# Kernel tuning notes

Measured on AMD Instinct MI355X. Metric: run time of the kernel, lower is better.

## Reference

```python
import jax, jax.numpy as jnp
import numpy as np

S, N, D, F = 32, 128, 256, 516
TRI = (N - 1) * N // 2  # fact(n-1) = n(n-1)/2 lower-triangular edge slots


def _mlp_readout(y, W0, b0, W1, b1, W2, b2):
    # standard MLPReadout with L=2 halving layers + final linear
    y = jax.nn.relu(y @ W0.T + b0)
    y = jax.nn.relu(y @ W1.T + b1)
    return y @ W2.T + b2


def _gru(xs, h0, Wih, Whh, bih, bhh):
    # xs: (S, T, Din); torch.nn.GRUCell math, scanned over time
    def step(h, x_t):
        gi = x_t @ Wih.T + bih
        gh = h @ Whh.T + bhh
        i_r, i_z, i_n = jnp.split(gi, 3, axis=-1)
        h_r, h_z, h_n = jnp.split(gh, 3, axis=-1)
        r = jax.nn.sigmoid(i_r + h_r)
        z = jax.nn.sigmoid(i_z + h_z)
        n = jnp.tanh(i_n + r * h_n)
        h_new = (1.0 - z) * n + z * h
        return h_new, h_new
    _, out = jax.lax.scan(step, h0, jnp.swapaxes(xs, 0, 1))
    return jnp.swapaxes(out, 0, 1)  # (S, T, D)


def setup_inputs() -> dict:
    key = jax.random.key(0)
    ks = jax.random.split(key, 16)
    def nrm(k, shape, s=0.05):
        return (jax.random.normal(k, shape) * s).astype(jnp.float32)
    return {
        'x': jax.random.uniform(ks[0], (S, N, F), dtype=jnp.float32),
        'con': jax.random.uniform(ks[1], (S, TRI, 2), dtype=jnp.float32),
        'z_ph': jax.random.uniform(ks[2], (D,), minval=-1.0, maxval=1.0, dtype=jnp.float32),
        'init_ph': jax.random.uniform(ks[3], (D,), minval=-1.0, maxval=1.0, dtype=jnp.float32),
        'cc_W0': nrm(ks[4], (D, 2 * D)), 'cc_b0': jnp.zeros((D,), jnp.float32),
        'cc_W1': nrm(ks[5], (D // 2, D)), 'cc_b1': jnp.zeros((D // 2,), jnp.float32),
        'cc_W2': nrm(ks[6], (D, D // 2)), 'cc_b2': jnp.zeros((D,), jnp.float32),
        'er_W0': nrm(ks[7], (D, 2 * D)), 'er_b0': jnp.zeros((D,), jnp.float32),
        'er_W1': nrm(ks[8], (D // 2, D)), 'er_b1': jnp.zeros((D // 2,), jnp.float32),
        'er_W2': nrm(ks[9], (2, D // 2)), 'er_b2': jnp.zeros((2,), jnp.float32),
        'rr_W': nrm(ks[10], (D, F)), 'rr_b': jnp.zeros((D,), jnp.float32),
        'dec_Wih': nrm(ks[11], (3 * D, D)), 'dec_Whh': nrm(ks[12], (3 * D, D)),
        'dec_bih': jnp.zeros((3 * D,), jnp.float32), 'dec_bhh': jnp.zeros((3 * D,), jnp.float32),
        'upd_Wih': nrm(ks[13], (3 * D, D)), 'upd_Whh': nrm(ks[14], (3 * D, D)),
        'upd_bih': jnp.zeros((3 * D,), jnp.float32), 'upd_bhh': jnp.zeros((3 * D,), jnp.float32),
    }


def reference(x, con, z_ph, init_ph, cc_W0, cc_b0, cc_W1, cc_b1, cc_W2, cc_b2,
              er_W0, er_b0, er_W1, er_b1, er_W2, er_b2, rr_W, rr_b,
              dec_Wih, dec_Whh, dec_bih, dec_bhh, upd_Wih, upd_Whh, upd_bih, upd_bhh):
    Sb = x.shape[0]
    Nm1 = x.shape[1] - 1
    # initial content = compact_content([z ; init]) (same for every sample)
    c0 = _mlp_readout(jnp.concatenate([z_ph, init_ph])[None, :],
                      cc_W0, cc_b0, cc_W1, cc_b1, cc_W2, cc_b2)
    c0 = jnp.broadcast_to(c0, (Sb, D))
    # update-model input stream depends only on data x[:, 1:] -> precompute
    rnninp = jax.nn.relu(jnp.einsum('snf,df->snd', x[:, 1:], rr_W) + rr_b)  # (S, N-1, D)
    h0 = jnp.zeros((Sb, D), x.dtype)
    u_out = _gru(rnninp, h0, upd_Wih, upd_Whh, upd_bih, upd_bhh)            # (S, N-1, D)
    # decoder consumes content0 then the first N-2 update outputs
    content_seq = jnp.concatenate([c0[:, None], u_out[:, :-1]], axis=1)     # (S, N-1, D)
    mem = _gru(content_seq, h0, dec_Wih, dec_Whh, dec_bih, dec_bhh)         # (S, N-1, D)
    # step i emits edges (j, i) for j <= i; flatten lower triangle (static indices)
    i_idx = np.repeat(np.arange(Nm1), np.arange(1, Nm1 + 1))
    j_idx = np.concatenate([np.arange(i + 1) for i in range(Nm1)])
    edge_rep = jnp.concatenate([mem[:, j_idx], mem[:, i_idx]], axis=-1)     # (S, TRI, 2D)
    logits = _mlp_readout(edge_rep, er_W0, er_b0, er_W1, er_b1, er_W2, er_b2)
    p = jax.nn.softmax(logits, axis=-1)                                     # (S, TRI, 2)
    # F.binary_cross_entropy with torch's log clamp at -100
    bce = -(con * jnp.clip(jnp.log(p), -100.0, None)
            + (1.0 - con) * jnp.clip(jnp.log1p(-p), -100.0, None))
    return jnp.sum(bce, axis=1)  # (S, 2) negative log-likelihood per class slot
```

## Files before the change

### kernel.cpp

```cpp
#include <hip/hip_runtime.h>
#include <cstddef>

#define S_ 32
#define NM1 127
#define D_ 256
#define F_ 516
#define TRI_ 8128
#define G_ 768
#define M_ (S_ * NM1)

typedef __bf16 v8bf __attribute__((ext_vector_type(8)));
typedef float v4f __attribute__((ext_vector_type(4)));

__device__ __forceinline__ unsigned short f2bf(float f) {
    unsigned int u = __float_as_uint(f);
    unsigned int r = (u + 0x7FFFu + ((u >> 16) & 1u)) >> 16;
    return (unsigned short)r;
}

__device__ __forceinline__ void store4bf(unsigned short* p, float4 v) {
    ushort4 q;
    q.x = f2bf(v.x); q.y = f2bf(v.y); q.z = f2bf(v.z); q.w = f2bf(v.w);
    *(ushort4*)p = q;
}

__device__ __forceinline__ v8bf u4_to_v8bf(uint4 u) {
    union { uint4 u; v8bf v; } x; x.u = u; return x.v;
}

__device__ __forceinline__ float sigmoidf_(float x) { return 1.f / (1.f + __expf(-x)); }

__device__ __forceinline__ float fast_tanh(float x) {
    float ax = fabsf(x);
    float e = __expf(2.f * ax);
    float t = 1.f - 2.f / (e + 1.f);
    return copysignf(t, x);
}

__global__ __launch_bounds__(1024) void c0_kernel(
    const float* __restrict__ z_ph, const float* __restrict__ init_ph,
    const float* __restrict__ W0, const float* __restrict__ b0,
    const float* __restrict__ W1, const float* __restrict__ b1,
    const float* __restrict__ W2, const float* __restrict__ b2,
    float* __restrict__ c0_out, float* __restrict__ out_zero)
{
    __shared__ float v[512];
    __shared__ float h0[256];
    __shared__ float h1[128];
    __shared__ float red[4][256];
    __shared__ float red1[8][128];
    const int t = threadIdx.x;
    if (t < 512) v[t] = (t < 256) ? z_ph[t] : init_ph[t - 256];
    if (t < 64) out_zero[t] = 0.f;
    __syncthreads();
    {
        int row = t & 255, part = t >> 8;
        const float* w = W0 + (size_t)row * 512 + part * 128;
        const float* vv = v + part * 128;
        float a = 0.f;
        for (int k = 0; k < 128; ++k) a += w[k] * vv[k];
        red[part][row] = a;
    }
    __syncthreads();
    if (t < 256) {
        float a = b0[t] + red[0][t] + red[1][t] + red[2][t] + red[3][t];
        h0[t] = fmaxf(a, 0.f);
    }
    __syncthreads();
    {
        int row = t & 127, part = t >> 7;
        const float* w = W1 + (size_t)row * 256 + part * 32;
        const float* vv = h0 + part * 32;
        float a = 0.f;
        for (int k = 0; k < 32; ++k) a += w[k] * vv[k];
        red1[part][row] = a;
    }
    __syncthreads();
    if (t < 128) {
        float a = b1[t];
        for (int p = 0; p < 8; ++p) a += red1[p][t];
        h1[t] = fmaxf(a, 0.f);
    }
    __syncthreads();
    {
        int row = t & 255, part = t >> 8;
        const float* w = W2 + (size_t)row * 128 + part * 32;
        const float* vv = h1 + part * 32;
        float a = 0.f;
        for (int k = 0; k < 32; ++k) a += w[k] * vv[k];
        red[part][row] = a;
    }
    __syncthreads();
    if (t < 256) c0_out[t] = b2[t] + red[0][t] + red[1][t] + red[2][t] + red[3][t];
}

__device__ __forceinline__ void do_packfrag(const float* __restrict__ W,
                                            uint4* __restrict__ wbuf, int idx)
{
    if (idx >= 48 * 8 * 64) return;
    int ct = idx >> 9;
    int rem = idx & 511;
    int kk = rem >> 6;
    int lane = rem & 63;
    int lr = lane & 15, quad = lane >> 4;
    const float* src = W + (size_t)(ct * 16 + lr) * 256 + kk * 32 + quad * 8;
    unsigned int wd[4];
#pragma unroll
    for (int i = 0; i < 4; ++i)
        wd[i] = (unsigned int)f2bf(src[2 * i]) | ((unsigned int)f2bf(src[2 * i + 1]) << 16);
    uint4 v; v.x = wd[0]; v.y = wd[1]; v.z = wd[2]; v.w = wd[3];
    wbuf[idx] = v;
}

__device__ __forceinline__ void do_cvt(const float* __restrict__ src,
                                       unsigned short* __restrict__ dst,
                                       int idx, int N, int K, int lds_, int off, int ldd)
{
    if (idx >= N * ldd) return;
    int n = idx / ldd, k = idx - n * ldd;
    float v = (k < K) ? src[(size_t)n * lds_ + off + k] : 0.f;
    dst[idx] = f2bf(v);
}

#define PREP_BLOCKS 2888

__global__ __launch_bounds__(256) void prep_all(
    const float* __restrict__ upd_Whh, uint4* __restrict__ wfU,
    const float* __restrict__ dec_Whh, uint4* __restrict__ wfD,
    const float* __restrict__ rr_W, unsigned short* __restrict__ rwbf,
    const float* __restrict__ upd_Wih, unsigned short* __restrict__ uwbf,
    const float* __restrict__ dec_Wih, unsigned short* __restrict__ dwbf,
    const float* __restrict__ er_W0, unsigned short* __restrict__ w0bf,
    const float* __restrict__ er_W1, unsigned short* __restrict__ w1bf)
{
    int bid = blockIdx.x;
    const int tid = threadIdx.x;
    if (bid < 96) { do_packfrag(upd_Whh, wfU, bid * 256 + tid); return; }
    bid -= 96;
    if (bid < 96) { do_packfrag(dec_Whh, wfD, bid * 256 + tid); return; }
    bid -= 96;
    if (bid < 520) { do_cvt(rr_W, rwbf, bid * 256 + tid, 256, 516, 516, 0, 520); return; }
    bid -= 520;
    if (bid < 768) { do_cvt(upd_Wih, uwbf, bid * 256 + tid, 768, 256, 256, 0, 256); return; }
    bid -= 768;
    if (bid < 768) { do_cvt(dec_Wih, dwbf, bid * 256 + tid, 768, 256, 256, 0, 256); return; }
    bid -= 768;
    if (bid < 256) { do_cvt(er_W0, w0bf, bid * 256 + tid, 256, 256, 512, 0, 256); return; }
    bid -= 256;
    if (bid < 256) { do_cvt(er_W0, w0bf + 256 * 256, bid * 256 + tid, 256, 256, 512, 256, 256); return; }
    bid -= 256;
    do_cvt(er_W1, w1bf, bid * 256 + tid, 128, 256, 256, 0, 256);
}

__global__ __launch_bounds__(256) void gemm_mfma(
    const float* __restrict__ A, const unsigned short* __restrict__ B,
    const float* __restrict__ bias, const float* __restrict__ c0,
    float* __restrict__ C, float* __restrict__ C2,
    int M, int N, int K, int lda, int ldb, int mode, int act, int split)
{
    __shared__ __align__(16) unsigned short As[64 * 128];
    __shared__ __align__(16) unsigned short Bs[64 * 128];
    const int tid = threadIdx.x;
    const int m0 = blockIdx.x * 64, n0 = blockIdx.y * 64;
    const int wave = tid >> 6, lane = tid & 63;
    const int lr = lane & 15, quad = lane >> 4;

    v4f acc[4];
    const v4f z4 = {0.f, 0.f, 0.f, 0.f};
#pragma unroll
    for (int nt = 0; nt < 4; ++nt) acc[nt] = z4;

    for (int k0 = 0; k0 < K; k0 += 128) {
        for (int idx = tid; idx < 64 * 32; idx += 256) {
            int r = idx >> 5, kq = idx & 31;
            int k = k0 + kq * 4;
            int m = m0 + r; if (m > M - 1) m = M - 1;
            float4 a = {0.f, 0.f, 0.f, 0.f};
            if (k < K) {
                const float* Ar;
                if (mode == 1) {
                    int ss = m / 127, tt = m - ss * 127;
                    Ar = A + (size_t)(ss * 128 + tt + 1) * lda;
                } else if (mode == 2) {
                    int tt = m % 127;
                    Ar = (tt == 0) ? c0 : (A + (size_t)(m - 1) * lda);
                } else {
                    Ar = A + (size_t)m * lda;
                }
                a = *(const float4*)&Ar[k];
            }
            store4bf(&As[r * 128 + (((kq >> 1) ^ (r & 7)) << 3) + ((kq & 1) << 2)], a);
        }
        for (int idx = tid; idx < 64 * 16; idx += 256) {
            int c = idx >> 4, kb = idx & 15;
            int k = k0 + kb * 8;
            int n = n0 + c;
            uint4 bv = {0u, 0u, 0u, 0u};
            if (k < K) bv = *(const uint4*)&B[(size_t)n * ldb + k];
            *(uint4*)&Bs[c * 128 + ((kb ^ (c & 7)) << 3)] = bv;
        }
        __syncthreads();
        const int row = wave * 16 + lr;
        const int rem = K - k0;
        const int kkm = (rem >= 128) ? 4 : ((rem + 31) >> 5);
        for (int kk = 0; kk < kkm; ++kk) {
            const v8bf af = *(const v8bf*)&As[row * 128 + ((((kk << 2) + quad) ^ (row & 7)) << 3)];
#pragma unroll
            for (int nt = 0; nt < 4; ++nt) {
                const int col = nt * 16 + lr;
                const v8bf bf = *(const v8bf*)&Bs[col * 128 + ((((kk << 2) + quad) ^ (col & 7)) << 3)];
                acc[nt] = __builtin_amdgcn_mfma_f32_16x16x32_bf16(af, bf, acc[nt], 0, 0, 0);
            }
        }
        __syncthreads();
    }
#pragma unroll
    for (int nt = 0; nt < 4; ++nt) {
        const int col = n0 + nt * 16 + lr;
#pragma unroll
        for (int r = 0; r < 4; ++r) {
            const int row = m0 + wave * 16 + quad * 4 + r;
            if (row < M) {
                float v = acc[nt][r];
                if (split) {
                    if (col < 256) C[(size_t)row * 256 + col] = v;
                    else C2[(size_t)row * 256 + (col - 256)] = v + bias[col - 256];
                } else {
                    if (bias) v += bias[col];
                    if (act) v = fmaxf(v, 0.f);
                    C[(size_t)row * N + col] = v;
                }
            }
        }
    }
}

__global__ __launch_bounds__(512, 2) void gru_scan6(
    const float* __restrict__ gi, const uint4* __restrict__ wf,
    const float* __restrict__ bhh, float* __restrict__ outp, int T)
{
    const int s = blockIdx.x, tid = threadIdx.x;
    const int w = tid >> 6, lane = tid & 63;
    const int quad = lane >> 4;
    __shared__ unsigned int hbuf[2][128];
    __shared__ float dred[768];

    uint4 wfr[6][8];
#pragma unroll
    for (int c = 0; c < 6; ++c)
#pragma unroll
        for (int kk = 0; kk < 8; ++kk)
            wfr[c][kk] = wf[((((w * 6 + c) * 8) + kk) << 6) | lane];

    float br = 0.f, bz = 0.f, bn = 0.f;
    float g_r = 0.f, g_z = 0.f, g_n = 0.f;
    const float* g0 = gi + (size_t)s * T * G_;
    float* o0 = outp + (size_t)s * T * D_;
    float h = 0.f;
    if (tid < 256) {
        br = bhh[tid]; bz = bhh[256 + tid]; bn = bhh[512 + tid];
        g_r = g0[tid]; g_z = g0[256 + tid]; g_n = g0[512 + tid];
    }
    if (tid < 128) { hbuf[0][tid] = 0u; hbuf[1][tid] = 0u; }

    v4f acc[6];
    const v4f z4 = {0.f, 0.f, 0.f, 0.f};
#pragma unroll
    for (int c = 0; c < 6; ++c) acc[c] = z4;
    __syncthreads();

    for (int t = 0; t < T; ++t) {
        float ngr = 0.f, ngz = 0.f, ngn = 0.f;
        if (tid < 256 && t + 1 < T) {
            const float* gn_ = g0 + (size_t)(t + 1) * G_;
            ngr = gn_[tid]; ngz = gn_[256 + tid]; ngn = gn_[512 + tid];
        }
        const unsigned int* hq = hbuf[t & 1];
#pragma unroll
        for (int kk = 0; kk < 8; ++kk) {
            const v8bf af = *(const v8bf*)&hq[kk * 16 + quad * 4];
#pragma unroll
            for (int c = 0; c < 6; ++c)
                acc[c] = __builtin_amdgcn_mfma_f32_16x16x32_bf16(
                    af, u4_to_v8bf(wfr[c][kk]), acc[c], 0, 0, 0);
        }
        if (lane < 16) {
#pragma unroll
            for (int c = 0; c < 6; ++c)
                dred[(w * 6 + c) * 16 + lane] = acc[c][0];
        }
#pragma unroll
        for (int c = 0; c < 6; ++c) acc[c] = z4;
        __syncthreads();
        if (tid < 256) {
            const float rg = sigmoidf_(g_r + dred[tid] + br);
            const float zg = sigmoidf_(g_z + dred[256 + tid] + bz);
            const float ng = fast_tanh(g_n + rg * (dred[512 + tid] + bn));
            const float hnew = ng + zg * (h - ng);
            h = hnew;
            o0[(size_t)t * D_ + tid] = hnew;
            const float ho = __shfl_xor(hnew, 1);
            if ((tid & 1) == 0)
                hbuf[(t + 1) & 1][tid >> 1] =
                    (unsigned int)f2bf(hnew) | ((unsigned int)f2bf(ho) << 16);
            g_r = ngr; g_z = ngz; g_n = ngn;
        }
        __syncthreads();
    }
}

__global__ __launch_bounds__(256) void edge_kernel(
    const float* __restrict__ Amat, const float* __restrict__ Bmat,
    const unsigned short* __restrict__ w1bf, const float* __restrict__ b1,
    const float* __restrict__ W2, const float* __restrict__ b2,
    const float* __restrict__ con, float* __restrict__ out)
{
    __shared__ __align__(16) unsigned short h1s[64 * 256];
    __shared__ int ijs[128];
    __shared__ float redw[4][2];
    const int tid = threadIdx.x;
    const int s = blockIdx.y;
    const int e0 = blockIdx.x * 64;

    if (tid < 64) {
        int e = e0 + tid;
        int i = (int)((sqrtf(8.f * (float)e + 1.f) - 1.f) * 0.5f);
        while (((i + 1) * (i + 2)) / 2 <= e) ++i;
        while ((i * (i + 1)) / 2 > e) --i;
        ijs[tid * 2] = i;
        ijs[tid * 2 + 1] = e - (i * (i + 1)) / 2;
    }
    __syncthreads();

    for (int idx = tid; idx < 64 * 64; idx += 256) {
        int e = idx >> 6, k4 = idx & 63;
        int i = ijs[e * 2], j = ijs[e * 2 + 1];
        float4 a = ((const float4*)(Amat + ((size_t)s * NM1 + j) * D_))[k4];
        float4 b = ((const float4*)(Bmat + ((size_t)s * NM1 + i) * D_))[k4];
        float4 hv;
        hv.x = fmaxf(a.x + b.x, 0.f);
        hv.y = fmaxf(a.y + b.y, 0.f);
        hv.z = fmaxf(a.z + b.z, 0.f);
        hv.w = fmaxf(a.w + b.w, 0.f);
        int pc = (k4 >> 1) ^ (e & 7);
        store4bf(&h1s[e * 256 + (pc << 3) + ((k4 & 1) << 2)], hv);
    }
    __syncthreads();

    const int wave = tid >> 6, lane = tid & 63;
    const int lr = lane & 15, quad = lane >> 4;
    const int row = wave * 16 + lr;

    v4f acc[8];
    const v4f vzero = {0.f, 0.f, 0.f, 0.f};
#pragma unroll
    for (int nt = 0; nt < 8; ++nt) acc[nt] = vzero;

#pragma unroll
    for (int kt = 0; kt < 8; ++kt) {
        const int c = kt * 4 + quad;
        const int pc = c ^ (row & 7);
        const v8bf afrag = *reinterpret_cast<const v8bf*>(&h1s[row * 256 + (pc << 3)]);
        const int ko = kt * 32 + quad * 8;
#pragma unroll
        for (int nt = 0; nt < 8; ++nt) {
            const v8bf bfrag = *reinterpret_cast<const v8bf*>(&w1bf[(size_t)(nt * 16 + lr) * D_ + ko]);
            acc[nt] = __builtin_amdgcn_mfma_f32_16x16x32_bf16(afrag, bfrag, acc[nt], 0, 0, 0);
        }
    }

    float w20[8], w21[8], b1v[8];
#pragma unroll
    for (int nt = 0; nt < 8; ++nt) {
        int oc = nt * 16 + lr;
        w20[nt] = W2[oc];
        w21[nt] = W2[128 + oc];
        b1v[nt] = b1[oc];
    }
    const float cb20 = b2[0], cb21 = b2[1];
    float bsum0 = 0.f, bsum1 = 0.f;
#pragma unroll
    for (int r = 0; r < 4; ++r) {
        float l0 = 0.f, l1 = 0.f;
#pragma unroll
        for (int nt = 0; nt < 8; ++nt) {
            float h2 = fmaxf(acc[nt][r] + b1v[nt], 0.f);
            l0 += h2 * w20[nt];
            l1 += h2 * w21[nt];
        }
#pragma unroll
        for (int d = 1; d < 16; d <<= 1) {
            l0 += __shfl_xor(l0, d);
            l1 += __shfl_xor(l1, d);
        }
        if (lr == 0) {
            int e = e0 + wave * 16 + quad * 4 + r;
            l0 += cb20; l1 += cb21;
            float mx = fmaxf(l0, l1);
            float lse = mx + logf(__expf(l0 - mx) + __expf(l1 - mx));
            float lp0 = fmaxf(l0 - lse, -100.f);
            float lp1 = fmaxf(l1 - lse, -100.f);
            float c0v = con[((size_t)s * TRI_ + e) * 2];
            float c1v = con[((size_t)s * TRI_ + e) * 2 + 1];
            bsum0 -= c0v * lp0 + (1.f - c0v) * lp1;
            bsum1 -= c1v * lp1 + (1.f - c1v) * lp0;
        }
    }
#pragma unroll
    for (int d = 1; d < 64; d <<= 1) {
        bsum0 += __shfl_xor(bsum0, d);
        bsum1 += __shfl_xor(bsum1, d);
    }
    if (lane == 0) { redw[wave][0] = bsum0; redw[wave][1] = bsum1; }
    __syncthreads();
    if (tid == 0) {
        float t0 = redw[0][0] + redw[1][0] + redw[2][0] + redw[3][0];
        float t1 = redw[0][1] + redw[1][1] + redw[2][1] + redw[3][1];
        atomicAdd(&out[s * 2], t0);
        atomicAdd(&out[s * 2 + 1], t1);
    }
}

extern "C" void kernel_launch(void* const* d_in, const int* in_sizes, int n_in,
                              void* d_out, int out_size, void* d_ws, size_t ws_size,
                              hipStream_t stream)
{
    (void)in_sizes; (void)n_in; (void)out_size; (void)ws_size;
    const float* x        = (const float*)d_in[0];
    const float* con      = (const float*)d_in[1];
    const float* z_ph     = (const float*)d_in[2];
    const float* init_ph  = (const float*)d_in[3];
    const float* cc_W0    = (const float*)d_in[4];
    const float* cc_b0    = (const float*)d_in[5];
    const float* cc_W1    = (const float*)d_in[6];
    const float* cc_b1    = (const float*)d_in[7];
    const float* cc_W2    = (const float*)d_in[8];
    const float* cc_b2    = (const float*)d_in[9];
    const float* er_W0    = (const float*)d_in[10];
    const float* er_b0    = (const float*)d_in[11];
    const float* er_W1    = (const float*)d_in[12];
    const float* er_b1    = (const float*)d_in[13];
    const float* er_W2    = (const float*)d_in[14];
    const float* er_b2    = (const float*)d_in[15];
    const float* rr_W     = (const float*)d_in[16];
    const float* rr_b     = (const float*)d_in[17];
    const float* dec_Wih  = (const float*)d_in[18];
    const float* dec_Whh  = (const float*)d_in[19];
    const float* dec_bih  = (const float*)d_in[20];
    const float* dec_bhh  = (const float*)d_in[21];
    const float* upd_Wih  = (const float*)d_in[22];
    const float* upd_Whh  = (const float*)d_in[23];
    const float* upd_bih  = (const float*)d_in[24];
    const float* upd_bhh  = (const float*)d_in[25];
    float* out = (float*)d_out;

    float* ws = (float*)d_ws;
    float* c0v  = ws;
    float* gi   = ws + 256;
    float* bufA = gi + (size_t)M_ * G_;
    float* bufB = bufA + (size_t)M_ * D_;
    float* memb = bufB + (size_t)M_ * D_;
    unsigned short* w1bf = (unsigned short*)(memb + (size_t)M_ * D_);
    unsigned short* rwbf = w1bf + 128 * 256;
    unsigned short* uwbf = rwbf + 256 * 520;
    unsigned short* dwbf = uwbf + 768 * 256;
    unsigned short* w0bf = dwbf + 768 * 256;
    uint4* wfU = (uint4*)(((size_t)(w0bf + 512 * 256) + 15) & ~(size_t)15);
    uint4* wfD = wfU + 48 * 8 * 64;

    c0_kernel<<<1, 1024, 0, stream>>>(z_ph, init_ph, cc_W0, cc_b0, cc_W1, cc_b1,
                                      cc_W2, cc_b2, c0v, out);
    prep_all<<<PREP_BLOCKS, 256, 0, stream>>>(upd_Whh, wfU, dec_Whh, wfD,
                                              rr_W, rwbf, upd_Wih, uwbf,
                                              dec_Wih, dwbf, er_W0, w0bf,
                                              er_W1, w1bf);
    gemm_mfma<<<dim3((M_ + 63) / 64, 256 / 64), 256, 0, stream>>>(
        x, rwbf, rr_b, nullptr, bufA, nullptr, M_, 256, 516, 516, 520, 1, 1, 0);
    gemm_mfma<<<dim3((M_ + 63) / 64, 768 / 64), 256, 0, stream>>>(
        bufA, uwbf, upd_bih, nullptr, gi, nullptr, M_, 768, 256, 256, 256, 0, 0, 0);
    gru_scan6<<<S_, 512, 0, stream>>>(gi, wfU, upd_bhh, bufB, NM1);
    gemm_mfma<<<dim3((M_ + 63) / 64, 768 / 64), 256, 0, stream>>>(
        bufB, dwbf, dec_bih, c0v, gi, nullptr, M_, 768, 256, 256, 256, 2, 0, 0);
    gru_scan6<<<S_, 512, 0, stream>>>(gi, wfD, dec_bhh, memb, NM1);
    gemm_mfma<<<dim3((M_ + 63) / 64, 512 / 64), 256, 0, stream>>>(
        memb, w0bf, er_b0, nullptr, bufA, bufB, M_, 512, 256, 256, 256, 0, 0, 1);
    edge_kernel<<<dim3(TRI_ / 64, S_), 256, 0, stream>>>(
        bufA, bufB, w1bf, er_b1, er_W2, er_b2, con, out);
}
```

Measured before the change: 682.9 us.

## Keep edge-MLP weights in registers and store split GEMM outputs as bf16

```diff
diff --git a/kernel.cpp b/kernel.cpp
--- a/kernel.cpp
+++ b/kernel.cpp
@@ -27,6 +27,9 @@
 __device__ __forceinline__ v8bf u4_to_v8bf(uint4 u) {
     union { uint4 u; v8bf v; } x; x.u = u; return x.v;
 }
+
+__device__ __forceinline__ float bflo(unsigned int u) { return __uint_as_float(u << 16); }
+__device__ __forceinline__ float bfhi(unsigned int u) { return __uint_as_float(u & 0xffff0000u); }
 
 __device__ __forceinline__ float sigmoidf_(float x) { return 1.f / (1.f + __expf(-x)); }
 
@@ -95,9 +98,10 @@
 }
 
 __device__ __forceinline__ void do_packfrag(const float* __restrict__ W,
-                                            uint4* __restrict__ wbuf, int idx)
-{
-    if (idx >= 48 * 8 * 64) return;
+                                            uint4* __restrict__ wbuf, int idx,
+                                            int ntiles)
+{
+    if (idx >= ntiles * 8 * 64) return;
     int ct = idx >> 9;
     int rem = idx & 511;
     int kk = rem >> 6;
@@ -122,23 +126,25 @@
     dst[idx] = f2bf(v);
 }
 
-#define PREP_BLOCKS 2888
+#define PREP_BLOCKS 2776
 
 __global__ __launch_bounds__(256) void prep_all(
     const float* __restrict__ upd_Whh, uint4* __restrict__ wfU,
     const float* __restrict__ dec_Whh, uint4* __restrict__ wfD,
+    const float* __restrict__ er_W1, uint4* __restrict__ w1f,
     const float* __restrict__ rr_W, unsigned short* __restrict__ rwbf,
     const float* __restrict__ upd_Wih, unsigned short* __restrict__ uwbf,
     const float* __restrict__ dec_Wih, unsigned short* __restrict__ dwbf,
-    const float* __restrict__ er_W0, unsigned short* __restrict__ w0bf,
-    const float* __restrict__ er_W1, unsigned short* __restrict__ w1bf)
+    const float* __restrict__ er_W0, unsigned short* __restrict__ w0bf)
 {
     int bid = blockIdx.x;
     const int tid = threadIdx.x;
-    if (bid < 96) { do_packfrag(upd_Whh, wfU, bid * 256 + tid); return; }
+    if (bid < 96) { do_packfrag(upd_Whh, wfU, bid * 256 + tid, 48); return; }
     bid -= 96;
-    if (bid < 96) { do_packfrag(dec_Whh, wfD, bid * 256 + tid); return; }
+    if (bid < 96) { do_packfrag(dec_Whh, wfD, bid * 256 + tid, 48); return; }
     bid -= 96;
+    if (bid < 16) { do_packfrag(er_W1, w1f, bid * 256 + tid, 8); return; }
+    bid -= 16;
     if (bid < 520) { do_cvt(rr_W, rwbf, bid * 256 + tid, 256, 516, 516, 0, 520); return; }
     bid -= 520;
     if (bid < 768) { do_cvt(upd_Wih, uwbf, bid * 256 + tid, 768, 256, 256, 0, 256); return; }
@@ -147,9 +153,7 @@
     bid -= 768;
     if (bid < 256) { do_cvt(er_W0, w0bf, bid * 256 + tid, 256, 256, 512, 0, 256); return; }
     bid -= 256;
-    if (bid < 256) { do_cvt(er_W0, w0bf + 256 * 256, bid * 256 + tid, 256, 256, 512, 256, 256); return; }
-    bid -= 256;
-    do_cvt(er_W1, w1bf, bid * 256 + tid, 128, 256, 256, 0, 256);
+    do_cvt(er_W0, w0bf + 256 * 256, bid * 256 + tid, 256, 256, 512, 256, 256);
 }
 
 __global__ __launch_bounds__(256) void gemm_mfma(
@@ -223,8 +227,11 @@
             if (row < M) {
                 float v = acc[nt][r];
                 if (split) {
-                    if (col < 256) C[(size_t)row * 256 + col] = v;
-                    else C2[(size_t)row * 256 + (col - 256)] = v + bias[col - 256];
+                    if (col < 256)
+                        ((unsigned short*)C)[(size_t)row * 256 + col] = f2bf(v);
+                    else
+                        ((unsigned short*)C2)[(size_t)row * 256 + (col - 256)] =
+                            f2bf(v + bias[col - 256]);
                 } else {
                     if (bias) v += bias[col];
                     if (act) v = fmaxf(v, 0.f);
@@ -309,18 +316,33 @@
     }
 }
 
-__global__ __launch_bounds__(256) void edge_kernel(
-    const float* __restrict__ Amat, const float* __restrict__ Bmat,
-    const unsigned short* __restrict__ w1bf, const float* __restrict__ b1,
+__global__ __launch_bounds__(256, 3) void edge_kernel2(
+    const unsigned short* __restrict__ Abf, const unsigned short* __restrict__ Bbf,
+    const uint4* __restrict__ w1f, const float* __restrict__ b1,
     const float* __restrict__ W2, const float* __restrict__ b2,
     const float* __restrict__ con, float* __restrict__ out)
 {
     __shared__ __align__(16) unsigned short h1s[64 * 256];
     __shared__ int ijs[128];
-    __shared__ float redw[4][2];
+    __shared__ float part[4][64][2];
     const int tid = threadIdx.x;
     const int s = blockIdx.y;
     const int e0 = blockIdx.x * 64;
+    const int wave = tid >> 6, lane = tid & 63;
+    const int lr = lane & 15, quad = lane >> 4;
+
+    uint4 wfr[2][8];
+#pragma unroll
+    for (int c = 0; c < 2; ++c)
+#pragma unroll
+        for (int kk = 0; kk < 8; ++kk)
+            wfr[c][kk] = w1f[((((wave * 2 + c) * 8) + kk) << 6) | lane];
+
+    const int ca = wave * 32 + lr, cb = wave * 32 + 16 + lr;
+    const float b1a = b1[ca], b1b = b1[cb];
+    const float w20a = W2[ca], w20b = W2[cb];
+    const float w21a = W2[128 + ca], w21b = W2[128 + cb];
+    const float cb20 = b2[0], cb21 = b2[1];
 
     if (tid < 64) {
         int e = e0 + tid;
@@ -332,92 +354,95 @@
     }
     __syncthreads();
 
-    for (int idx = tid; idx < 64 * 64; idx += 256) {
-        int e = idx >> 6, k4 = idx & 63;
-        int i = ijs[e * 2], j = ijs[e * 2 + 1];
-        float4 a = ((const float4*)(Amat + ((size_t)s * NM1 + j) * D_))[k4];
-        float4 b = ((const float4*)(Bmat + ((size_t)s * NM1 + i) * D_))[k4];
-        float4 hv;
-        hv.x = fmaxf(a.x + b.x, 0.f);
-        hv.y = fmaxf(a.y + b.y, 0.f);
-        hv.z = fmaxf(a.z + b.z, 0.f);
-        hv.w = fmaxf(a.w + b.w, 0.f);
-        int pc = (k4 >> 1) ^ (e & 7);
-        store4bf(&h1s[e * 256 + (pc << 3) + ((k4 & 1) << 2)], hv);
-    }
-    __syncthreads();
-
-    const int wave = tid >> 6, lane = tid & 63;
-    const int lr = lane & 15, quad = lane >> 4;
-    const int row = wave * 16 + lr;
-
-    v4f acc[8];
-    const v4f vzero = {0.f, 0.f, 0.f, 0.f};
-#pragma unroll
-    for (int nt = 0; nt < 8; ++nt) acc[nt] = vzero;
-
-#pragma unroll
-    for (int kt = 0; kt < 8; ++kt) {
-        const int c = kt * 4 + quad;
-        const int pc = c ^ (row & 7);
-        const v8bf afrag = *reinterpret_cast<const v8bf*>(&h1s[row * 256 + (pc << 3)]);
-        const int ko = kt * 32 + quad * 8;
-#pragma unroll
-        for (int nt = 0; nt < 8; ++nt) {
-            const v8bf bfrag = *reinterpret_cast<const v8bf*>(&w1bf[(size_t)(nt * 16 + lr) * D_ + ko]);
-            acc[nt] = __builtin_amdgcn_mfma_f32_16x16x32_bf16(afrag, bfrag, acc[nt], 0, 0, 0);
-        }
-    }
-
-    float w20[8], w21[8], b1v[8];
-#pragma unroll
-    for (int nt = 0; nt < 8; ++nt) {
-        int oc = nt * 16 + lr;
-        w20[nt] = W2[oc];
-        w21[nt] = W2[128 + oc];
-        b1v[nt] = b1[oc];
-    }
-    const float cb20 = b2[0], cb21 = b2[1];
-    float bsum0 = 0.f, bsum1 = 0.f;
-#pragma unroll
-    for (int r = 0; r < 4; ++r) {
-        float l0 = 0.f, l1 = 0.f;
-#pragma unroll
-        for (int nt = 0; nt < 8; ++nt) {
-            float h2 = fmaxf(acc[nt][r] + b1v[nt], 0.f);
-            l0 += h2 * w20[nt];
-            l1 += h2 * w21[nt];
-        }
-#pragma unroll
-        for (int d = 1; d < 16; d <<= 1) {
-            l0 += __shfl_xor(l0, d);
-            l1 += __shfl_xor(l1, d);
-        }
-        if (lr == 0) {
-            int e = e0 + wave * 16 + quad * 4 + r;
-            l0 += cb20; l1 += cb21;
-            float mx = fmaxf(l0, l1);
-            float lse = mx + logf(__expf(l0 - mx) + __expf(l1 - mx));
-            float lp0 = fmaxf(l0 - lse, -100.f);
-            float lp1 = fmaxf(l1 - lse, -100.f);
-            float c0v = con[((size_t)s * TRI_ + e) * 2];
-            float c1v = con[((size_t)s * TRI_ + e) * 2 + 1];
-            bsum0 -= c0v * lp0 + (1.f - c0v) * lp1;
-            bsum1 -= c1v * lp1 + (1.f - c1v) * lp0;
-        }
-    }
-#pragma unroll
-    for (int d = 1; d < 64; d <<= 1) {
-        bsum0 += __shfl_xor(bsum0, d);
-        bsum1 += __shfl_xor(bsum1, d);
-    }
-    if (lane == 0) { redw[wave][0] = bsum0; redw[wave][1] = bsum1; }
-    __syncthreads();
-    if (tid == 0) {
-        float t0 = redw[0][0] + redw[1][0] + redw[2][0] + redw[3][0];
-        float t1 = redw[0][1] + redw[1][1] + redw[2][1] + redw[3][1];
-        atomicAdd(&out[s * 2], t0);
-        atomicAdd(&out[s * 2 + 1], t1);
+    {
+        const unsigned short* Aro = Abf + (size_t)s * NM1 * 256;
+        const unsigned short* Bro = Bbf + (size_t)s * NM1 * 256;
+#pragma unroll
+        for (int it = 0; it < 8; ++it) {
+            int idx = tid + it * 256;
+            int e = idx >> 5, k8 = idx & 31;
+            int i = ijs[2 * e], j = ijs[2 * e + 1];
+            uint4 av = *(const uint4*)&Aro[(size_t)j * 256 + k8 * 8];
+            uint4 bv = *(const uint4*)&Bro[(size_t)i * 256 + k8 * 8];
+            unsigned int rr[4];
+#pragma unroll
+            for (int wd = 0; wd < 4; ++wd) {
+                unsigned int aw = (&av.x)[wd], bw = (&bv.x)[wd];
+                float lo = fmaxf(bflo(aw) + bflo(bw), 0.f);
+                float hi = fmaxf(bfhi(aw) + bfhi(bw), 0.f);
+                rr[wd] = (unsigned int)f2bf(lo) | ((unsigned int)f2bf(hi) << 16);
+            }
+            uint4 hv; hv.x = rr[0]; hv.y = rr[1]; hv.z = rr[2]; hv.w = rr[3];
+            *(uint4*)&h1s[e * 256 + ((k8 ^ (e & 7)) << 3)] = hv;
+        }
+    }
+    __syncthreads();
+
+    v4f acc[4][2];
+    const v4f z4 = {0.f, 0.f, 0.f, 0.f};
+#pragma unroll
+    for (int rt = 0; rt < 4; ++rt) { acc[rt][0] = z4; acc[rt][1] = z4; }
+
+#pragma unroll
+    for (int kk = 0; kk < 8; ++kk) {
+        v8bf af[4];
+#pragma unroll
+        for (int rt = 0; rt < 4; ++rt) {
+            const int row = rt * 16 + lr;
+            af[rt] = *(const v8bf*)&h1s[row * 256 + ((((kk << 2) + quad) ^ (row & 7)) << 3)];
+        }
+#pragma unroll
+        for (int rt = 0; rt < 4; ++rt) {
+            acc[rt][0] = __builtin_amdgcn_mfma_f32_16x16x32_bf16(
+                af[rt], u4_to_v8bf(wfr[0][kk]), acc[rt][0], 0, 0, 0);
+            acc[rt][1] = __builtin_amdgcn_mfma_f32_16x16x32_bf16(
+                af[rt], u4_to_v8bf(wfr[1][kk]), acc[rt][1], 0, 0, 0);
+        }
+    }
+
+#pragma unroll
+    for (int rt = 0; rt < 4; ++rt) {
+#pragma unroll
+        for (int r = 0; r < 4; ++r) {
+            float h2a = fmaxf(acc[rt][0][r] + b1a, 0.f);
+            float h2b = fmaxf(acc[rt][1][r] + b1b, 0.f);
+            float p0 = h2a * w20a + h2b * w20b;
+            float p1 = h2a * w21a + h2b * w21b;
+#pragma unroll
+            for (int d = 1; d < 16; d <<= 1) {
+                p0 += __shfl_xor(p0, d);
+                p1 += __shfl_xor(p1, d);
+            }
+            if (lr == 0) {
+                int e = rt * 16 + quad * 4 + r;
+                part[wave][e][0] = p0;
+                part[wave][e][1] = p1;
+            }
+        }
+    }
+    __syncthreads();
+
+    if (tid < 64) {
+        float l0 = part[0][tid][0] + part[1][tid][0] + part[2][tid][0] + part[3][tid][0] + cb20;
+        float l1 = part[0][tid][1] + part[1][tid][1] + part[2][tid][1] + part[3][tid][1] + cb21;
+        int e = e0 + tid;
+        float mx = fmaxf(l0, l1);
+        float lse = mx + logf(__expf(l0 - mx) + __expf(l1 - mx));
+        float lp0 = fmaxf(l0 - lse, -100.f);
+        float lp1 = fmaxf(l1 - lse, -100.f);
+        float c0v = con[((size_t)s * TRI_ + e) * 2];
+        float c1v = con[((size_t)s * TRI_ + e) * 2 + 1];
+        float bsum0 = -(c0v * lp0 + (1.f - c0v) * lp1);
+        float bsum1 = -(c1v * lp1 + (1.f - c1v) * lp0);
+#pragma unroll
+        for (int d = 1; d < 64; d <<= 1) {
+            bsum0 += __shfl_xor(bsum0, d);
+            bsum1 += __shfl_xor(bsum1, d);
+        }
+        if (tid == 0) {
+            atomicAdd(&out[s * 2], bsum0);
+            atomicAdd(&out[s * 2 + 1], bsum1);
+        }
     }
 }
 
@@ -460,20 +485,20 @@
     float* bufA = gi + (size_t)M_ * G_;
     float* bufB = bufA + (size_t)M_ * D_;
     float* memb = bufB + (size_t)M_ * D_;
-    unsigned short* w1bf = (unsigned short*)(memb + (size_t)M_ * D_);
-    unsigned short* rwbf = w1bf + 128 * 256;
+    unsigned short* rwbf = (unsigned short*)(memb + (size_t)M_ * D_);
     unsigned short* uwbf = rwbf + 256 * 520;
     unsigned short* dwbf = uwbf + 768 * 256;
     unsigned short* w0bf = dwbf + 768 * 256;
     uint4* wfU = (uint4*)(((size_t)(w0bf + 512 * 256) + 15) & ~(size_t)15);
     uint4* wfD = wfU + 48 * 8 * 64;
+    uint4* w1f = wfD + 48 * 8 * 64;
 
     c0_kernel<<<1, 1024, 0, stream>>>(z_ph, init_ph, cc_W0, cc_b0, cc_W1, cc_b1,
                                       cc_W2, cc_b2, c0v, out);
     prep_all<<<PREP_BLOCKS, 256, 0, stream>>>(upd_Whh, wfU, dec_Whh, wfD,
+                                              er_W1, w1f,
                                               rr_W, rwbf, upd_Wih, uwbf,
-                                              dec_Wih, dwbf, er_W0, w0bf,
-                                              er_W1, w1bf);
+                                              dec_Wih, dwbf, er_W0, w0bf);
     gemm_mfma<<<dim3((M_ + 63) / 64, 256 / 64), 256, 0, stream>>>(
         x, rwbf, rr_b, nullptr, bufA, nullptr, M_, 256, 516, 516, 520, 1, 1, 0);
     gemm_mfma<<<dim3((M_ + 63) / 64, 768 / 64), 256, 0, stream>>>(
@@ -484,6 +509,7 @@
     gru_scan6<<<S_, 512, 0, stream>>>(gi, wfD, dec_bhh, memb, NM1);
     gemm_mfma<<<dim3((M_ + 63) / 64, 512 / 64), 256, 0, stream>>>(
         memb, w0bf, er_b0, nullptr, bufA, bufB, M_, 512, 256, 256, 256, 0, 0, 1);
-    edge_kernel<<<dim3(TRI_ / 64, S_), 256, 0, stream>>>(
-        bufA, bufB, w1bf, er_b1, er_W2, er_b2, con, out);
-}
+    edge_kernel2<<<dim3(TRI_ / 64, S_), 256, 0, stream>>>(
+        (const unsigned short*)bufA, (const unsigned short*)bufB,
+        w1f, er_b1, er_W2, er_b2, con, out);
+}
```

Result: faster. 615.7 us (-9.8%).
